# Optimization experiments

Hardware: AMD Instinct MI355X
Metric: run time of the kernel (lower is better)

The kernel has to match this reference:

```python
import jax, jax.numpy as jnp
import numpy as np

H = 4
NEG_SLOPE = 0.2
N_P, N_A = 100000, 100000
E = 500000
L = 200000
F_IN, F_HID, F_OUT = 128, 128, 64


def setup_inputs() -> dict:
    key = jax.random.key(0)
    ks = jax.random.split(key, 32)
    s = 0.1  # weight init scale
    inp = {
        'x_paper': jax.random.normal(ks[0], (N_P, F_IN), jnp.float32),
        'x_author': jax.random.normal(ks[1], (N_A, F_IN), jnp.float32),
        'ei_pa': jax.random.randint(ks[2], (2, E), 0, N_P, jnp.int32),
        'ei_ap': jax.random.randint(ks[3], (2, E), 0, N_A, jnp.int32),
        'edge_label_index': jax.random.randint(ks[4], (2, L), 0, N_P, jnp.int32),
        # layer 1 params
        'p1W': s * jax.random.normal(ks[5], (F_IN, F_HID), jnp.float32),
        'p1b': jnp.zeros((F_HID,), jnp.float32),
        'a1W': s * jax.random.normal(ks[6], (F_IN, F_HID), jnp.float32),
        'a1b': jnp.zeros((F_HID,), jnp.float32),
        's1pa': s * jax.random.normal(ks[7], (H, F_HID // H), jnp.float32),
        'd1pa': s * jax.random.normal(ks[8], (H, F_HID // H), jnp.float32),
        's1ap': s * jax.random.normal(ks[9], (H, F_HID // H), jnp.float32),
        'd1ap': s * jax.random.normal(ks[10], (H, F_HID // H), jnp.float32),
        'k1W': s * jax.random.normal(ks[11], (F_HID, F_HID), jnp.float32),
        'k1b': jnp.zeros((F_HID,), jnp.float32),
        'q1': s * jax.random.normal(ks[12], (F_HID,), jnp.float32),
        # layer 2 params
        'p2W': s * jax.random.normal(ks[13], (F_HID, F_OUT), jnp.float32),
        'p2b': jnp.zeros((F_OUT,), jnp.float32),
        'a2W': s * jax.random.normal(ks[14], (F_HID, F_OUT), jnp.float32),
        'a2b': jnp.zeros((F_OUT,), jnp.float32),
        's2pa': s * jax.random.normal(ks[15], (H, F_OUT // H), jnp.float32),
        'd2pa': s * jax.random.normal(ks[16], (H, F_OUT // H), jnp.float32),
        's2ap': s * jax.random.normal(ks[17], (H, F_OUT // H), jnp.float32),
        'd2ap': s * jax.random.normal(ks[18], (H, F_OUT // H), jnp.float32),
        'k2W': s * jax.random.normal(ks[19], (F_OUT, F_OUT), jnp.float32),
        'k2b': jnp.zeros((F_OUT,), jnp.float32),
        'q2': s * jax.random.normal(ks[20], (F_OUT,), jnp.float32),
    }
    return inp


def _edge_attn(h_src, h_dst, src, dst, a_src, a_dst, num_dst):
    # h_*: [N, H, D]; a_*: [H, D]. Per-edge node-level GAT-style attention.
    alpha = (jnp.einsum('nhd,hd->nh', h_src, a_src)[src]
             + jnp.einsum('nhd,hd->nh', h_dst, a_dst)[dst])  # [E, H]
    alpha = jnp.where(alpha >= 0, alpha, NEG_SLOPE * alpha)  # leaky_relu
    amax = jax.ops.segment_max(alpha, dst, num_segments=num_dst)
    amax = jnp.where(jnp.isfinite(amax), amax, 0.0)
    ex = jnp.exp(alpha - amax[dst])
    denom = jax.ops.segment_sum(ex, dst, num_segments=num_dst)
    w = ex / (denom[dst] + 1e-16)
    out = jax.ops.segment_sum(h_src[src] * w[:, :, None], dst, num_segments=num_dst)
    return jax.nn.relu(out).reshape(num_dst, -1)  # [N_dst, H*D]


def _group(xs, q, kW, kb):
    # Semantic-level attention over metapaths (PyG HANConv `group`).
    out = jnp.stack(xs)  # [M, N, F]
    score = (q * jnp.tanh(out @ kW + kb).mean(axis=1)).sum(-1)  # [M]
    attn = jax.nn.softmax(score)
    return (attn[:, None, None] * out).sum(0)


def _han_layer(x_p, x_a, ei_pa, ei_ap, pW, pb, aW, ab, s_pa, d_pa, s_ap, d_ap, kW, kb, q):
    D = pW.shape[1] // H
    h_p = (x_p @ pW + pb).reshape(-1, H, D)
    h_a = (x_a @ aW + ab).reshape(-1, H, D)
    out_a = _edge_attn(h_p, h_a, ei_pa[0], ei_pa[1], s_pa, d_pa, h_a.shape[0])
    out_p = _edge_attn(h_a, h_p, ei_ap[0], ei_ap[1], s_ap, d_ap, h_p.shape[0])
    z_p = _group([out_p], q, kW, kb)
    z_a = _group([out_a], q, kW, kb)
    return z_p, z_a


def reference(x_paper, x_author, ei_pa, ei_ap, edge_label_index,
              p1W, p1b, a1W, a1b, s1pa, d1pa, s1ap, d1ap, k1W, k1b, q1,
              p2W, p2b, a2W, a2b, s2pa, d2pa, s2ap, d2ap, k2W, k2b, q2):
    z_p, z_a = _han_layer(x_paper, x_author, ei_pa, ei_ap,
                          p1W, p1b, a1W, a1b, s1pa, d1pa, s1ap, d1ap, k1W, k1b, q1)
    z_p, z_a = _han_layer(z_p, z_a, ei_pa, ei_ap,
                          p2W, p2b, a2W, a2b, s2pa, d2pa, s2ap, d2ap, k2W, k2b, q2)
    src = z_p[edge_label_index[0]]
    dst = z_a[edge_label_index[1]]
    return (src * dst).sum(axis=-1)  # [L]
```

## Files before the change

### kernel.cpp

```cpp
#include <hip/hip_runtime.h>


#define HEADS 4

typedef _Float16 f16x8 __attribute__((ext_vector_type(8)));
typedef _Float16 f16x4 __attribute__((ext_vector_type(4)));
typedef float    f32x4 __attribute__((ext_vector_type(4)));

__device__ __forceinline__ float leaky02(float a) {
    return a >= 0.f ? a : 0.2f * a;
}

__device__ __forceinline__ void prep_one(const float* W, _Float16* Wf, int M, int o) {
    const int NT = M / 16;
    const int v = o & 7, lane = (o >> 3) & 63, jt = o >> 9;
    const int t = jt / NT, j = jt % NT;
    const int k = t * 32 + (lane >> 4) * 8 + v;
    const int n = j * 16 + (lane & 15);
    Wf[o] = (_Float16)W[k * M + n];
}

__global__ __launch_bounds__(256) void prep_w4(
    const float* __restrict__ W1, _Float16* __restrict__ Wf1,
    const float* __restrict__ W2, _Float16* __restrict__ Wf2,
    const float* __restrict__ W3, _Float16* __restrict__ Wf3,
    const float* __restrict__ W4, _Float16* __restrict__ Wf4) {
    int o = blockIdx.x * 256 + threadIdx.x;
    if (o < 16384)       prep_one(W1, Wf1, 128, o);
    else if (o < 32768)  prep_one(W2, Wf2, 128, o - 16384);
    else if (o < 40960)  prep_one(W3, Wf3, 64, o - 32768);
    else if (o < 49152)  prep_one(W4, Wf4, 64, o - 40960);
}

template<int M, bool AHALF>
__global__ __launch_bounds__(256) void gemm_mfma_dual(
    const void* __restrict__ XA, const _Float16* __restrict__ WfA,
    const float* __restrict__ bA, _Float16* __restrict__ outA,
    const float* __restrict__ svA, const float* __restrict__ dvA,
    float* __restrict__ asA, float* __restrict__ adA,
    const void* __restrict__ XB, const _Float16* __restrict__ WfB,
    const float* __restrict__ bB, _Float16* __restrict__ outB,
    const float* __restrict__ svB, const float* __restrict__ dvB,
    float* __restrict__ asB, float* __restrict__ adB,
    int N, int nbHalf) {
    constexpr int NT = M / 16;
    constexpr int D  = M / HEADS;
    __shared__ _Float16 stage[4][16][M + 4];

    const bool second = blockIdx.x >= nbHalf;
    const void* __restrict__ X      = second ? XB : XA;
    const _Float16* __restrict__ Wf = second ? WfB : WfA;
    const float* __restrict__ b     = second ? bB : bA;
    _Float16* __restrict__ out      = second ? outB : outA;
    const float* __restrict__ sv    = second ? svB : svA;
    const float* __restrict__ dv    = second ? dvB : dvA;
    float* __restrict__ asb         = second ? asB : asA;
    float* __restrict__ adb         = second ? adB : adA;
    const int brow = second ? blockIdx.x - nbHalf : blockIdx.x;

    const int wave = threadIdx.x >> 6;
    const int lane = threadIdx.x & 63;
    const int row0 = (brow * 4 + wave) * 16;
    const int m    = lane & 15;
    const int quad = lane >> 4;

    f32x4 acc[NT];
    #pragma unroll
    for (int j = 0; j < NT; ++j) acc[j] = (f32x4){0.f, 0.f, 0.f, 0.f};

    int arow = row0 + m;
    if (arow >= N) arow = N - 1;

    #pragma unroll
    for (int t = 0; t < 4; ++t) {
        const int k0 = t * 32 + quad * 8;
        f16x8 a;
        if (AHALF) {
            a = *(const f16x8*)((const _Float16*)X + (size_t)arow * 128 + k0);
        } else {
            const float* xp = (const float*)X + (size_t)arow * 128 + k0;
            float4 v0 = *(const float4*)xp;
            float4 v1 = *(const float4*)(xp + 4);
            a = (f16x8){(_Float16)v0.x, (_Float16)v0.y, (_Float16)v0.z, (_Float16)v0.w,
                        (_Float16)v1.x, (_Float16)v1.y, (_Float16)v1.z, (_Float16)v1.w};
        }
        #pragma unroll
        for (int j = 0; j < NT; ++j) {
            f16x8 bf = *(const f16x8*)(Wf + ((size_t)(t * NT + j) * 64 + lane) * 8);
            acc[j] = __builtin_amdgcn_mfma_f32_16x16x32_f16(a, bf, acc[j], 0, 0, 0);
        }
    }

    #pragma unroll
    for (int j = 0; j < NT; ++j) {
        const float bias = b[j * 16 + m];
        #pragma unroll
        for (int r = 0; r < 4; ++r)
            stage[wave][quad * 4 + r][j * 16 + m] = (_Float16)(acc[j][r] + bias);
    }

    {
        const int r  = lane >> 2;
        const int hh = lane & 3;
        float ps = 0.f, pd = 0.f;
        #pragma unroll
        for (int j = 0; j < D / 4; ++j) {
            f16x4 v4 = *(const f16x4*)(&stage[wave][r][hh * D + 4 * j]);
            float4 s4 = *(const float4*)(sv + hh * D + 4 * j);
            float4 d4 = *(const float4*)(dv + hh * D + 4 * j);
            const float v0 = (float)v4[0], v1 = (float)v4[1],
                        v2 = (float)v4[2], v3 = (float)v4[3];
            ps += v0 * s4.x + v1 * s4.y + v2 * s4.z + v3 * s4.w;
            pd += v0 * d4.x + v1 * d4.y + v2 * d4.z + v3 * d4.w;
        }
        const int grow = row0 + r;
        if (grow < N) {
            asb[(size_t)grow * HEADS + hh] = ps;
            adb[(size_t)grow * HEADS + hh] = pd;
        }
    }

    constexpr int LPR = M / 4;
    constexpr int RPI = 64 / LPR;
    const int lr = lane % LPR;
    const int rq = lane / LPR;
    #pragma unroll
    for (int i = 0; i < 16 / RPI; ++i) {
        const int rr = i * RPI + rq;
        const int grow = row0 + rr;
        if (grow < N) {
            f16x4 v = *(const f16x4*)(&stage[wave][rr][lr * 4]);
            *(f16x4*)(out + (size_t)grow * M + lr * 4) = v;
        }
    }
}

__global__ __launch_bounds__(256) void hist_dual(
    const int* __restrict__ dst_pa, const int* __restrict__ dst_ap,
    int* __restrict__ counts, int N, int E) {
    const int eg = blockIdx.x * 256 + threadIdx.x;
    if (eg >= 2 * E) return;
    const int idx = (eg < E) ? dst_pa[eg] : (N + dst_ap[eg - E]);
    atomicAdd(counts + idx, 1);
}

__global__ __launch_bounds__(256) void scan_blk(
    const int* __restrict__ in, int* __restrict__ out,
    int* __restrict__ bsum, int N) {
    __shared__ int sh[256];
    const int base = blockIdx.x * 1024 + threadIdx.x * 4;
    int v[4]; int s = 0;
    #pragma unroll
    for (int j = 0; j < 4; ++j) { v[j] = (base + j < N) ? in[base + j] : 0; s += v[j]; }
    sh[threadIdx.x] = s;
    __syncthreads();
    for (int off = 1; off < 256; off <<= 1) {
        int t = (threadIdx.x >= off) ? sh[threadIdx.x - off] : 0;
        __syncthreads();
        sh[threadIdx.x] += t;
        __syncthreads();
    }
    int run = sh[threadIdx.x] - s;
    #pragma unroll
    for (int j = 0; j < 4; ++j) {
        if (base + j < N) out[base + j] = run;
        run += v[j];
    }
    if (threadIdx.x == 255) bsum[blockIdx.x] = sh[255];
}

__global__ __launch_bounds__(256) void scan_sums(int* __restrict__ bsum, int nb) {
    __shared__ int sh[256];
    int v = (threadIdx.x < nb) ? bsum[threadIdx.x] : 0;
    sh[threadIdx.x] = v;
    __syncthreads();
    for (int off = 1; off < 256; off <<= 1) {
        int t = (threadIdx.x >= off) ? sh[threadIdx.x - off] : 0;
        __syncthreads();
        sh[threadIdx.x] += t;
        __syncthreads();
    }
    if (threadIdx.x < nb) bsum[threadIdx.x] = sh[threadIdx.x] - v;
}

__global__ __launch_bounds__(256) void scan_add(
    int* __restrict__ out, const int* __restrict__ bsum, int N) {
    const int base = blockIdx.x * 1024 + threadIdx.x * 4;
    const int add = bsum[blockIdx.x];
    #pragma unroll
    for (int j = 0; j < 4; ++j)
        if (base + j < N) out[base + j] += add;
}

__global__ __launch_bounds__(256) void scatter_dual(
    const int* __restrict__ src_pa, const int* __restrict__ dst_pa,
    const int* __restrict__ src_ap, const int* __restrict__ dst_ap,
    const int* __restrict__ offsets, int* __restrict__ cursor,
    int* __restrict__ perm, int N, int E) {
    const int eg = blockIdx.x * 256 + threadIdx.x;
    if (eg >= 2 * E) return;
    int idx, val;
    if (eg < E) { idx = dst_pa[eg];         val = src_pa[eg]; }
    else        { idx = N + dst_ap[eg - E]; val = src_ap[eg - E]; }
    const int pos = offsets[idx] + atomicAdd(cursor + idx, 1);
    perm[pos] = val;
}

__global__ __launch_bounds__(256) void deg_hist(
    const int* __restrict__ cnt, int* __restrict__ bhist, int n) {
    __shared__ int lh[64];
    if (threadIdx.x < 64) lh[threadIdx.x] = 0;
    __syncthreads();
    for (int i = blockIdx.x * 256 + threadIdx.x; i < n; i += gridDim.x * 256) {
        int c = cnt[i]; if (c > 63) c = 63;
        atomicAdd(&lh[c], 1);
    }
    __syncthreads();
    if (threadIdx.x < 64) atomicAdd(&bhist[threadIdx.x], lh[threadIdx.x]);
}

__global__ __launch_bounds__(256) void deg_scatter(
    const int* __restrict__ cnt, int* __restrict__ bcur,
    int* __restrict__ order, int n) {
    __shared__ int lh[64];
    __shared__ int lbase[64];
    if (threadIdx.x < 64) lh[threadIdx.x] = 0;
    __syncthreads();
    const int i = blockIdx.x * 256 + threadIdx.x;
    int c = 0, lpos = 0;
    if (i < n) {
        c = cnt[i]; if (c > 63) c = 63;
        lpos = atomicAdd(&lh[c], 1);
    }
    __syncthreads();
    if (threadIdx.x < 64 && lh[threadIdx.x] > 0)
        lbase[threadIdx.x] = atomicAdd(&bcur[threadIdx.x], lh[threadIdx.x]);
    __syncthreads();
    if (i < n) order[lbase[c] + lpos] = i;
}

template<int F, int D>
__global__ __launch_bounds__(256) void csr_attn_agg_dual(
    const int* __restrict__ order,
    const int* __restrict__ perm, const int* __restrict__ offsets,
    const int* __restrict__ counts,
    const float* __restrict__ asrcP, const float* __restrict__ adstP,
    const _Float16* __restrict__ hP, _Float16* __restrict__ outA,
    const float* __restrict__ asrcA, const float* __restrict__ adstA,
    const _Float16* __restrict__ hA, _Float16* __restrict__ outP,
    int N) {
    constexpr int LPN = F / 4;
    const int gid  = blockIdx.x * 256 + threadIdx.x;
    const int slot = gid / LPN;
    const int lane = gid % LPN;
    if (slot >= 2 * N) return;
    const int node_g = order[slot];
    const bool second = node_g >= N;
    const int node = second ? node_g - N : node_g;
    const float* __restrict__ asrc    = second ? asrcA : asrcP;
    const float* __restrict__ adst    = second ? adstA : adstP;
    const _Float16* __restrict__ hsrc = second ? hA : hP;
    _Float16* __restrict__ out        = second ? outP : outA;

    const int start = offsets[node_g];
    const int cnt   = counts[node_g];
    const int f0 = lane * 4;
    const int h  = f0 / D;
    const float ad = adst[(size_t)node * HEADS + h];

    float den = 0.f;
    float4 acc = make_float4(0.f, 0.f, 0.f, 0.f);
    int i = 0;
    for (; i + 4 <= cnt; i += 4) {
        const int s0 = perm[start + i + 0];
        const int s1 = perm[start + i + 1];
        const int s2 = perm[start + i + 2];
        const int s3 = perm[start + i + 3];
        const float a0 = asrc[(size_t)s0 * HEADS + h];
        const float a1 = asrc[(size_t)s1 * HEADS + h];
        const float a2 = asrc[(size_t)s2 * HEADS + h];
        const float a3 = asrc[(size_t)s3 * HEADS + h];
        f16x4 h0 = *(const f16x4*)(hsrc + (size_t)s0 * F + f0);
        f16x4 h1 = *(const f16x4*)(hsrc + (size_t)s1 * F + f0);
        f16x4 h2 = *(const f16x4*)(hsrc + (size_t)s2 * F + f0);
        f16x4 h3 = *(const f16x4*)(hsrc + (size_t)s3 * F + f0);
        const float e0 = __expf(leaky02(a0 + ad));
        const float e1 = __expf(leaky02(a1 + ad));
        const float e2 = __expf(leaky02(a2 + ad));
        const float e3 = __expf(leaky02(a3 + ad));
        den += (e0 + e1) + (e2 + e3);
        acc.x += e0 * (float)h0[0] + e1 * (float)h1[0] + e2 * (float)h2[0] + e3 * (float)h3[0];
        acc.y += e0 * (float)h0[1] + e1 * (float)h1[1] + e2 * (float)h2[1] + e3 * (float)h3[1];
        acc.z += e0 * (float)h0[2] + e1 * (float)h1[2] + e2 * (float)h2[2] + e3 * (float)h3[2];
        acc.w += e0 * (float)h0[3] + e1 * (float)h1[3] + e2 * (float)h2[3] + e3 * (float)h3[3];
    }
    for (; i < cnt; ++i) {
        const int s = perm[start + i];
        const float a = leaky02(asrc[(size_t)s * HEADS + h] + ad);
        const float ex = __expf(a);
        den += ex;
        f16x4 hv = *(const f16x4*)(hsrc + (size_t)s * F + f0);
        acc.x += ex * (float)hv[0]; acc.y += ex * (float)hv[1];
        acc.z += ex * (float)hv[2]; acc.w += ex * (float)hv[3];
    }
    const float inv = 1.f / (den + 1e-16f);
    f16x4 o;
    o[0] = (_Float16)fmaxf(acc.x * inv, 0.f);
    o[1] = (_Float16)fmaxf(acc.y * inv, 0.f);
    o[2] = (_Float16)fmaxf(acc.z * inv, 0.f);
    o[3] = (_Float16)fmaxf(acc.w * inv, 0.f);
    *(f16x4*)(out + (size_t)node * F + f0) = o;
}

__global__ __launch_bounds__(256) void edge_dot(
    const int* __restrict__ eli, const _Float16* __restrict__ zp,
    const _Float16* __restrict__ za, float* __restrict__ out, int L) {
    constexpr int LPE = 16;
    const int gid  = blockIdx.x * blockDim.x + threadIdx.x;
    const int e    = gid / LPE;
    const int lane = gid % LPE;
    if (e >= L) return;
    const int p = eli[e], a = eli[(size_t)L + e];
    f16x4 pv = *(const f16x4*)(zp + (size_t)p * 64 + lane * 4);
    f16x4 av = *(const f16x4*)(za + (size_t)a * 64 + lane * 4);
    float s = (float)pv[0] * (float)av[0] + (float)pv[1] * (float)av[1]
            + (float)pv[2] * (float)av[2] + (float)pv[3] * (float)av[3];
    #pragma unroll
    for (int off = 8; off > 0; off >>= 1) s += __shfl_xor(s, off);
    if (lane == 0) out[e] = s;
}

static inline int cdiv(long long a, long long b) { return (int)((a + b - 1) / b); }

extern "C" void kernel_launch(void* const* d_in, const int* in_sizes, int n_in,
                              void* d_out, int out_size, void* d_ws, size_t ws_size,
                              hipStream_t stream) {
    const float* x_p  = (const float*)d_in[0];
    const float* x_a  = (const float*)d_in[1];
    const int* ei_pa  = (const int*)d_in[2];
    const int* ei_ap  = (const int*)d_in[3];
    const int* eli    = (const int*)d_in[4];
    const float* p1W = (const float*)d_in[5];
    const float* p1b = (const float*)d_in[6];
    const float* a1W = (const float*)d_in[7];
    const float* a1b = (const float*)d_in[8];
    const float* s1pa = (const float*)d_in[9];
    const float* d1pa = (const float*)d_in[10];
    const float* s1ap = (const float*)d_in[11];
    const float* d1ap = (const float*)d_in[12];
    const float* p2W = (const float*)d_in[16];
    const float* p2b = (const float*)d_in[17];
    const float* a2W = (const float*)d_in[18];
    const float* a2b = (const float*)d_in[19];
    const float* s2pa = (const float*)d_in[20];
    const float* d2pa = (const float*)d_in[21];
    const float* s2ap = (const float*)d_in[22];
    const float* d2ap = (const float*)d_in[23];

    const int NP = in_sizes[0] / 128;
    const int E  = in_sizes[2] / 2;
    const int L  = in_sizes[4] / 2;
    const int N  = NP;

    char* ws = (char*)d_ws;
    size_t off = 0;
    auto alloc = [&](size_t bytes) -> char* {
        char* p = ws + off;
        off += (bytes + 255) & ~(size_t)255;
        return p;
    };
    _Float16* h_p1   = (_Float16*)alloc((size_t)N * 128 * 2);
    _Float16* h_a1   = (_Float16*)alloc((size_t)N * 128 * 2);
    _Float16* out_p1 = (_Float16*)alloc((size_t)N * 128 * 2);
    _Float16* out_a1 = (_Float16*)alloc((size_t)N * 128 * 2);
    _Float16* h_p2   = (_Float16*)alloc((size_t)N * 64 * 2);
    _Float16* h_a2   = (_Float16*)alloc((size_t)N * 64 * 2);
    _Float16* out_p2 = (_Float16*)alloc((size_t)N * 64 * 2);
    _Float16* out_a2 = (_Float16*)alloc((size_t)N * 64 * 2);
    float* asrc_pa = (float*)alloc((size_t)N * HEADS * 4);
    float* adst_pa = (float*)alloc((size_t)N * HEADS * 4);
    float* asrc_ap = (float*)alloc((size_t)N * HEADS * 4);
    float* adst_ap = (float*)alloc((size_t)N * HEADS * 4);
    _Float16* Wf1p = (_Float16*)alloc(16384 * 2);
    _Float16* Wf1a = (_Float16*)alloc(16384 * 2);
    _Float16* Wf2p = (_Float16*)alloc(8192 * 2);
    _Float16* Wf2a = (_Float16*)alloc(8192 * 2);
    int* cnt2    = (int*)alloc((size_t)2 * N * 4);
    int* cursor2 = (int*)alloc((size_t)2 * N * 4);
    int* bhist   = (int*)alloc(256);
    int* off2    = (int*)alloc((size_t)2 * N * 4);
    int* perm2   = (int*)alloc((size_t)2 * E * 4);
    int* order2  = (int*)alloc((size_t)2 * N * 4);
    int* bsum    = (int*)alloc(256 * 4);

    const int* src_pa = ei_pa;
    const int* dst_pa = ei_pa + E;
    const int* src_ap = ei_ap;
    const int* dst_ap = ei_ap + E;

    const int N2 = 2 * N;
    const int nbScan = cdiv(N2, 1024);

    prep_w4<<<cdiv(49152, 256), 256, 0, stream>>>(p1W, Wf1p, a1W, Wf1a, p2W, Wf2p, a2W, Wf2a);
    hipMemsetAsync(cnt2, 0, ((size_t)4 * N + 64) * 4, stream);
    hist_dual<<<cdiv((long long)2 * E, 256), 256, 0, stream>>>(dst_pa, dst_ap, cnt2, N, E);
    scan_blk<<<nbScan, 256, 0, stream>>>(cnt2, off2, bsum, N2);
    scan_sums<<<1, 256, 0, stream>>>(bsum, nbScan);
    scan_add<<<nbScan, 256, 0, stream>>>(off2, bsum, N2);
    scatter_dual<<<cdiv((long long)2 * E, 256), 256, 0, stream>>>(
        src_pa, dst_pa, src_ap, dst_ap, off2, cursor2, perm2, N, E);
    deg_hist<<<256, 256, 0, stream>>>(cnt2, bhist, N2);
    scan_sums<<<1, 256, 0, stream>>>(bhist, 64);
    deg_scatter<<<cdiv(N2, 256), 256, 0, stream>>>(cnt2, bhist, order2, N2);

    const int nbHalf = cdiv(N, 64);

    gemm_mfma_dual<128, false><<<2 * nbHalf, 256, 0, stream>>>(
        x_p, Wf1p, p1b, h_p1, s1pa, d1ap, asrc_pa, adst_ap,
        x_a, Wf1a, a1b, h_a1, s1ap, d1pa, asrc_ap, adst_pa, N, nbHalf);
    csr_attn_agg_dual<128, 32><<<cdiv((long long)N2 * 32, 256), 256, 0, stream>>>(
        order2, perm2, off2, cnt2,
        asrc_pa, adst_pa, h_p1, out_a1,
        asrc_ap, adst_ap, h_a1, out_p1, N);

    gemm_mfma_dual<64, true><<<2 * nbHalf, 256, 0, stream>>>(
        out_p1, Wf2p, p2b, h_p2, s2pa, d2ap, asrc_pa, adst_ap,
        out_a1, Wf2a, a2b, h_a2, s2ap, d2pa, asrc_ap, adst_pa, N, nbHalf);
    csr_attn_agg_dual<64, 16><<<cdiv((long long)N2 * 16, 256), 256, 0, stream>>>(
        order2, perm2, off2, cnt2,
        asrc_pa, adst_pa, h_p2, out_a2,
        asrc_ap, adst_ap, h_a2, out_p2, N);

    edge_dot<<<cdiv((long long)L * 16, 256), 256, 0, stream>>>(
        eli, out_p2, out_a2, (float*)d_out, L);
}
```

Baseline: 465.2 us.

## Process two 16-row fragments per wave in dual MFMA GEMM to reuse weight loads

Each wave in the node-projection GEMM now handles 32 rows (two MFMA fragments) instead of 16. All A-operand rows are preloaded into registers, and each weight fragment loaded from global memory feeds two MFMAs, halving weight traffic per row. The grid shrinks to half as many blocks and the LDS staging buffer doubles. In exchange, register pressure rises and there are fewer blocks to hide latency.

```diff
diff --git a/kernel.cpp b/kernel.cpp
--- a/kernel.cpp
+++ b/kernel.cpp
@@ -45,7 +45,7 @@
     int N, int nbHalf) {
     constexpr int NT = M / 16;
     constexpr int D  = M / HEADS;
-    __shared__ _Float16 stage[4][16][M + 4];
+    __shared__ _Float16 stage[4][32][M + 4];
 
     const bool second = blockIdx.x >= nbHalf;
     const void* __restrict__ X      = second ? XB : XA;
@@ -60,47 +60,69 @@
 
     const int wave = threadIdx.x >> 6;
     const int lane = threadIdx.x & 63;
-    const int row0 = (brow * 4 + wave) * 16;
+    const int row0 = (brow * 4 + wave) * 32;
     const int m    = lane & 15;
     const int quad = lane >> 4;
 
-    f32x4 acc[NT];
-    #pragma unroll
-    for (int j = 0; j < NT; ++j) acc[j] = (f32x4){0.f, 0.f, 0.f, 0.f};
-
-    int arow = row0 + m;
-    if (arow >= N) arow = N - 1;
-
+    int ar[2];
+    ar[0] = row0 + m;       if (ar[0] >= N) ar[0] = N - 1;
+    ar[1] = row0 + 16 + m;  if (ar[1] >= N) ar[1] = N - 1;
+
+    f16x8 areg[2][4];
     #pragma unroll
     for (int t = 0; t < 4; ++t) {
         const int k0 = t * 32 + quad * 8;
-        f16x8 a;
-        if (AHALF) {
-            a = *(const f16x8*)((const _Float16*)X + (size_t)arow * 128 + k0);
-        } else {
-            const float* xp = (const float*)X + (size_t)arow * 128 + k0;
-            float4 v0 = *(const float4*)xp;
-            float4 v1 = *(const float4*)(xp + 4);
-            a = (f16x8){(_Float16)v0.x, (_Float16)v0.y, (_Float16)v0.z, (_Float16)v0.w,
-                        (_Float16)v1.x, (_Float16)v1.y, (_Float16)v1.z, (_Float16)v1.w};
+        #pragma unroll
+        for (int f = 0; f < 2; ++f) {
+            if (AHALF) {
+                areg[f][t] = *(const f16x8*)((const _Float16*)X + (size_t)ar[f] * 128 + k0);
+            } else {
+                const float* xp = (const float*)X + (size_t)ar[f] * 128 + k0;
+                float4 v0 = *(const float4*)xp;
+                float4 v1 = *(const float4*)(xp + 4);
+                areg[f][t] = (f16x8){(_Float16)v0.x, (_Float16)v0.y, (_Float16)v0.z, (_Float16)v0.w,
+                                     (_Float16)v1.x, (_Float16)v1.y, (_Float16)v1.z, (_Float16)v1.w};
+            }
         }
+    }
+
+    f32x4 acc[2][NT];
+    #pragma unroll
+    for (int f = 0; f < 2; ++f)
+        #pragma unroll
+        for (int j = 0; j < NT; ++j) acc[f][j] = (f32x4){0.f, 0.f, 0.f, 0.f};
+
+    #pragma unroll
+    for (int th = 0; th < 2; ++th) {
+        f16x8 wreg[2][NT];
+        #pragma unroll
+        for (int tt = 0; tt < 2; ++tt)
+            #pragma unroll
+            for (int j = 0; j < NT; ++j)
+                wreg[tt][j] = *(const f16x8*)(Wf + ((size_t)((th * 2 + tt) * NT + j) * 64 + lane) * 8);
+        #pragma unroll
+        for (int tt = 0; tt < 2; ++tt)
+            #pragma unroll
+            for (int f = 0; f < 2; ++f)
+                #pragma unroll
+                for (int j = 0; j < NT; ++j)
+                    acc[f][j] = __builtin_amdgcn_mfma_f32_16x16x32_f16(
+                        areg[f][th * 2 + tt], wreg[tt][j], acc[f][j], 0, 0, 0);
+    }
+
+    #pragma unroll
+    for (int f = 0; f < 2; ++f)
         #pragma unroll
         for (int j = 0; j < NT; ++j) {
-            f16x8 bf = *(const f16x8*)(Wf + ((size_t)(t * NT + j) * 64 + lane) * 8);
-            acc[j] = __builtin_amdgcn_mfma_f32_16x16x32_f16(a, bf, acc[j], 0, 0, 0);
+            const float bias = b[j * 16 + m];
+            #pragma unroll
+            for (int r = 0; r < 4; ++r)
+                stage[wave][f * 16 + quad * 4 + r][j * 16 + m] = (_Float16)(acc[f][j][r] + bias);
         }
-    }
-
-    #pragma unroll
-    for (int j = 0; j < NT; ++j) {
-        const float bias = b[j * 16 + m];
-        #pragma unroll
-        for (int r = 0; r < 4; ++r)
-            stage[wave][quad * 4 + r][j * 16 + m] = (_Float16)(acc[j][r] + bias);
-    }
-
-    {
-        const int r  = lane >> 2;
+
+    #pragma unroll
+    for (int f = 0; f < 2; ++f) {
+        const int r  = f * 16 + (lane >> 2);
         const int hh = lane & 3;
         float ps = 0.f, pd = 0.f;
         #pragma unroll
@@ -125,7 +147,7 @@
     const int lr = lane % LPR;
     const int rq = lane / LPR;
     #pragma unroll
-    for (int i = 0; i < 16 / RPI; ++i) {
+    for (int i = 0; i < 32 / RPI; ++i) {
         const int rr = i * RPI + rq;
         const int grow = row0 + rr;
         if (grow < N) {
@@ -413,7 +435,7 @@
     scan_sums<<<1, 256, 0, stream>>>(bhist, 64);
     deg_scatter<<<cdiv(N2, 256), 256, 0, stream>>>(cnt2, bhist, order2, N2);
 
-    const int nbHalf = cdiv(N, 64);
+    const int nbHalf = cdiv(N, 128);
 
     gemm_mfma_dual<128, false><<<2 * nbHalf, 256, 0, stream>>>(
         x_p, Wf1p, p1b, h_p1, s1pa, d1ap, asrc_pa, adst_ap,
```

Result: no change. 468.4 us (+0.7%).
